# Kernel optimization log

Measured on AMD Instinct MI355X. Metric: run time of the kernel, lower is better.

Reference implementation:

```python
import jax, jax.numpy as jnp
import numpy as np

BN_EPS = 1e-5


def grid_sample_bilinear(img, grid):
    """Torch F.grid_sample, mode=bilinear, padding_mode=zeros, align_corners=False.
    img: (B, C, H, W); grid: (B, N, 2) in [-1, 1] -> (B, C, N)."""
    B, C, H, W = img.shape
    x = ((grid[..., 0] + 1.0) * W - 1.0) * 0.5  # (B, N) pixel coords
    y = ((grid[..., 1] + 1.0) * H - 1.0) * 0.5
    x0 = jnp.floor(x)
    y0 = jnp.floor(y)
    x1 = x0 + 1.0
    y1 = y0 + 1.0
    wx1 = x - x0
    wx0 = 1.0 - wx1
    wy1 = y - y0
    wy0 = 1.0 - wy1
    img_flat = img.reshape(B, C, H * W)

    def corner(xi, yi, w):
        valid = (xi >= 0) & (xi <= W - 1) & (yi >= 0) & (yi <= H - 1)
        xi_c = jnp.clip(xi, 0, W - 1).astype(jnp.int32)
        yi_c = jnp.clip(yi, 0, H - 1).astype(jnp.int32)
        idx = yi_c * W + xi_c  # (B, N)
        vals = jnp.take_along_axis(img_flat, idx[:, None, :], axis=2)  # (B, C, N)
        return vals * (w * valid.astype(img.dtype))[:, None, :]

    return (corner(x0, y0, wx0 * wy0) + corner(x1, y0, wx1 * wy0)
            + corner(x0, y1, wx0 * wy1) + corner(x1, y1, wx1 * wy1))


def conv1x1(x, w, b):
    # x: (B, Cin, N), w: (Cout, Cin), b: (Cout,)
    return jnp.einsum('oi,bin->bon', w, x) + b[None, :, None]


def batchnorm1d_train(x, gamma, beta):
    # training-mode BN over (batch, length) per channel, biased variance
    mean = jnp.mean(x, axis=(0, 2), keepdims=True)
    var = jnp.mean((x - mean) ** 2, axis=(0, 2), keepdims=True)
    xn = (x - mean) * jax.lax.rsqrt(var + BN_EPS)
    return xn * gamma[None, :, None] + beta[None, :, None]


def setup_inputs() -> dict:
    key = jax.random.key(0)
    ks = jax.random.split(key, 12)
    B, N, CI, CP, H, W, R = 4, 16384, 256, 256, 64, 160, 4
    Cin = CI + CP
    Cb = CP // R

    def glorot(k, shape):
        fan_in = shape[1]
        return jax.random.normal(k, shape, dtype=jnp.float32) * (1.0 / np.sqrt(fan_in))

    return {
        'pts_img': jax.random.uniform(ks[0], (B, N, 2), dtype=jnp.float32, minval=-1.0, maxval=1.0),
        'img_feats': jax.random.normal(ks[1], (B, CI, H, W), dtype=jnp.float32),
        'pts_feats': jax.random.normal(ks[2], (B, CP, N), dtype=jnp.float32),
        'fusion_w': glorot(ks[3], (CP, Cin)),
        'fusion_b': jax.random.normal(ks[4], (CP,), dtype=jnp.float32) * 0.01,
        'bn_gamma': jnp.ones((CP,), dtype=jnp.float32),
        'bn_beta': jnp.zeros((CP,), dtype=jnp.float32),
        'ca1_w': glorot(ks[5], (Cb, CP)),
        'ca1_b': jax.random.normal(ks[6], (Cb,), dtype=jnp.float32) * 0.01,
        'ca2_w': glorot(ks[7], (CP, Cb)),
        'ca2_b': jax.random.normal(ks[8], (CP,), dtype=jnp.float32) * 0.01,
        'sa_w': glorot(ks[9], (Cb, CP)),
        'sa_b': jax.random.normal(ks[10], (Cb,), dtype=jnp.float32) * 0.01,
    }


def reference(pts_img, img_feats, pts_feats, fusion_w, fusion_b, bn_gamma, bn_beta,
              ca1_w, ca1_b, ca2_w, ca2_b, sa_w, sa_b):
    # grid_sample gather: (B, C_I, N)
    pts_wise_img_feats = grid_sample_bilinear(img_feats, pts_img)
    fusion = jnp.concatenate([pts_wise_img_feats, pts_feats], axis=1)  # (B, C_I+C_P, N)
    # fusion MLP: conv1x1 + BN + ReLU
    fusion = jax.nn.relu(batchnorm1d_train(conv1x1(fusion, fusion_w, fusion_b), bn_gamma, bn_beta))
    # spatial attention: max over channels of bottleneck conv, sigmoid gate
    spatial = jax.nn.sigmoid(jnp.max(conv1x1(fusion, sa_w, sa_b), axis=1, keepdims=True))
    fusion = spatial * fusion
    # channel attention: bottleneck MLP, global max-pool over points, sigmoid gate
    ca = conv1x1(jax.nn.relu(conv1x1(fusion, ca1_w, ca1_b)), ca2_w, ca2_b)  # (B, C_P, N)
    channel = jax.nn.sigmoid(jnp.max(ca, axis=2, keepdims=True))  # (B, C_P, 1)
    return channel * fusion
```

## Files before the change

### kernel.cpp

```cpp
#include <hip/hip_runtime.h>
#include <stdint.h>


typedef __attribute__((ext_vector_type(8))) short bf16x8;
typedef __attribute__((ext_vector_type(4))) float f32x4;

#define B_ 4
#define N_ 16384
#define H_ 64
#define W_ 160
#define HW_ (H_ * W_)
#define K_ 512

__device__ __forceinline__ float bf2f(unsigned short u) {
    union { unsigned int i; float f; } c; c.i = ((unsigned int)u) << 16; return c.f;
}
__device__ __forceinline__ unsigned short f2bf(float f) {
    union { float f; unsigned int i; } c; c.f = f;
    unsigned int u = c.i;
    return (unsigned short)((u + 0x7FFFu + ((u >> 16) & 1u)) >> 16);
}
__device__ __forceinline__ unsigned int fkey(float f) {
    union { float f; unsigned int u; int i; } c; c.f = f;
    return (c.i < 0) ? ~c.u : (c.u | 0x80000000u);
}
__device__ __forceinline__ float funkey(unsigned int k) {
    union { unsigned int u; float f; } c;
    c.u = (k & 0x80000000u) ? (k & 0x7FFFFFFFu) : ~k;
    return c.f;
}

__device__ __forceinline__ void async_copy16(void* lds, const void* g) {
#if defined(__has_builtin) && __has_builtin(__builtin_amdgcn_global_load_lds)
    __builtin_amdgcn_global_load_lds(
        (const __attribute__((address_space(1))) unsigned int*)g,
        (__attribute__((address_space(3))) unsigned int*)lds, 16, 0, 0);
#else
    *(uint4*)lds = *(const uint4*)g;
#endif
}

__global__ __launch_bounds__(256) void k_init(const float* __restrict__ fw,
                                              const float* __restrict__ saw,
                                              const float* __restrict__ c1w,
                                              const float* __restrict__ c2w,
                                              unsigned short* WfB, unsigned short* saB,
                                              unsigned short* ca1B, unsigned short* ca2B,
                                              float* buckets, unsigned int* camax) {
    int t = threadIdx.x;
    int j = blockIdx.x;
    if (j == 0) {
        for (int i = t; i < 16 * 512; i += 256) buckets[i] = 0.f;
        for (int i = t; i < 8 * 1024; i += 256) camax[i] = 0u;
    }
    int i = j * 256 + t;
    if (i < 131072) WfB[i] = f2bf(fw[i]);
    else if (i < 147456) saB[i - 131072] = f2bf(saw[i - 131072]);
    else if (i < 163840) ca1B[i - 147456] = f2bf(c1w[i - 147456]);
    else if (i < 180224) ca2B[i - 163840] = f2bf(c2w[i - 163840]);
}

__global__ __launch_bounds__(256, 3) void k_zimg(const unsigned short* __restrict__ WfB,
                                                 const float* __restrict__ img,
                                                 unsigned short* __restrict__ ZT) {
    __shared__ __align__(16) char smem[33792];
    unsigned short* At = (unsigned short*)smem;
    unsigned short* Bt = (unsigned short*)(smem + 16384);
    unsigned short* tile = (unsigned short*)smem;

    int t = threadIdx.x;
    int hw0 = blockIdx.x * 64, b = blockIdx.y;
    int w = t >> 6, lane = t & 63, quad = lane >> 4, l15 = lane & 15;

    const f32x4 fzero = {0.f, 0.f, 0.f, 0.f};
    f32x4 acc[4][4];
#pragma unroll
    for (int i = 0; i < 4; ++i)
#pragma unroll
        for (int j = 0; j < 4; ++j) acc[i][j] = fzero;

    for (int kt = 0; kt < 8; ++kt) {
        int k0 = kt * 32;
        __syncthreads();
#pragma unroll
        for (int q = 0; q < 4; ++q) {
            int row = q * 64 + (t >> 2);
            async_copy16(At + (size_t)q * 2048 + (size_t)t * 8,
                         WfB + (size_t)row * K_ + k0 + (t & 3) * 8);
        }
        {
            int c_local = t & 31, g = t >> 5;
            int c = k0 + c_local;
            const float* src = img + ((size_t)b * 256 + c) * (size_t)HW_ + hw0 + g * 8;
            float4 v0 = *(const float4*)(src + 0);
            float4 v1 = *(const float4*)(src + 4);
            unsigned short* dst = Bt + (size_t)(g * 8) * 40 + c_local;
            dst[0 * 40] = f2bf(v0.x); dst[1 * 40] = f2bf(v0.y);
            dst[2 * 40] = f2bf(v0.z); dst[3 * 40] = f2bf(v0.w);
            dst[4 * 40] = f2bf(v1.x); dst[5 * 40] = f2bf(v1.y);
            dst[6 * 40] = f2bf(v1.z); dst[7 * 40] = f2bf(v1.w);
        }
        __syncthreads();
        bf16x8 af[4], bv[4];
#pragma unroll
        for (int j = 0; j < 4; ++j)
            bv[j] = *(const bf16x8*)(Bt + (j * 16 + l15) * 40 + quad * 8);
#pragma unroll
        for (int i = 0; i < 4; ++i)
            af[i] = *(const bf16x8*)(At + (w * 64 + i * 16 + l15) * 32 + quad * 8);
#pragma unroll
        for (int i = 0; i < 4; ++i)
#pragma unroll
            for (int j = 0; j < 4; ++j)
                acc[i][j] = __builtin_amdgcn_mfma_f32_16x16x32_bf16(af[i], bv[j], acc[i][j], 0, 0, 0);
    }

    __syncthreads();
#pragma unroll
    for (int i = 0; i < 4; ++i) {
        int m = w * 64 + i * 16 + quad * 4;
#pragma unroll
        for (int j = 0; j < 4; ++j) {
            int n = j * 16 + l15;
            ushort4 o;
            o.x = f2bf(acc[i][j][0]);
            o.y = f2bf(acc[i][j][1]);
            o.z = f2bf(acc[i][j][2]);
            o.w = f2bf(acc[i][j][3]);
            *(ushort4*)(tile + n * 264 + m) = o;
        }
    }
    __syncthreads();
    unsigned short* Zb = ZT + ((size_t)b * HW_ + hw0) * 256;
#pragma unroll
    for (int pass = 0; pass < 8; ++pass) {
        int row = pass * 8 + (t >> 5);
        int col = (t & 31) * 8;
        *(uint4*)(Zb + (size_t)row * 256 + col) = *(const uint4*)(tile + row * 264 + col);
    }
}

__global__ __launch_bounds__(256, 4) void k_gemm1p(const unsigned short* __restrict__ WfB,
                                                   const float* __restrict__ pim,
                                                   const unsigned short* __restrict__ ZT,
                                                   const float* __restrict__ pts,
                                                   const float* __restrict__ fb,
                                                   unsigned short* __restrict__ Y,
                                                   float* __restrict__ buckets) {
    __shared__ __align__(16) char smem[38912];
    unsigned short* At = (unsigned short*)smem;
    unsigned short* Bt = (unsigned short*)(smem + 16384);
    unsigned short* tile = (unsigned short*)smem;
    uint4*  offs4 = (uint4*)(smem + 33792);
    float4* wts4  = (float4*)(smem + 34816);
    float* biasS = (float*)(smem + 35840);
    float* redS  = (float*)(smem + 36864);
    float* redQ  = (float*)(smem + 37888);

    int t = threadIdx.x;
    int n0 = blockIdx.x * 64, bb = blockIdx.y;
    int w = t >> 6, lane = t & 63, quad = lane >> 4, l15 = lane & 15;
    const unsigned short* Zb = ZT + (size_t)bb * HW_ * 256;

    if (t < 64) {
        float2 g2 = *(const float2*)(pim + (size_t)((size_t)bb * N_ + n0 + t) * 2);
        float x = (g2.x + 1.0f) * (0.5f * W_) - 0.5f;
        float y = (g2.y + 1.0f) * (0.5f * H_) - 0.5f;
        float xf = floorf(x), yf = floorf(y);
        float wx1 = x - xf, wx0 = 1.0f - wx1;
        float wy1 = y - yf, wy0 = 1.0f - wy1;
        int x0 = (int)xf, y0 = (int)yf;
        int x1 = x0 + 1, y1 = y0 + 1;
        float vx0 = (x0 >= 0 && x0 < W_) ? 1.f : 0.f;
        float vx1 = (x1 >= 0 && x1 < W_) ? 1.f : 0.f;
        float vy0 = (y0 >= 0 && y0 < H_) ? 1.f : 0.f;
        float vy1 = (y1 >= 0 && y1 < H_) ? 1.f : 0.f;
        int cx0 = min(max(x0, 0), W_ - 1), cx1 = min(max(x1, 0), W_ - 1);
        int cy0 = min(max(y0, 0), H_ - 1), cy1 = min(max(y1, 0), H_ - 1);
        uint4 o4;
        o4.x = (unsigned)(cy0 * W_ + cx0);
        o4.y = (unsigned)(cy0 * W_ + cx1);
        o4.z = (unsigned)(cy1 * W_ + cx0);
        o4.w = (unsigned)(cy1 * W_ + cx1);
        offs4[t] = o4;
        float4 w4;
        w4.x = wx0 * wy0 * vx0 * vy0;
        w4.y = wx1 * wy0 * vx1 * vy0;
        w4.z = wx0 * wy1 * vx0 * vy1;
        w4.w = wx1 * wy1 * vx1 * vy1;
        wts4[t] = w4;
    }
    biasS[t] = fb[t];

    const f32x4 fzero = {0.f, 0.f, 0.f, 0.f};
    f32x4 acc[4][4];
#pragma unroll
    for (int i = 0; i < 4; ++i)
#pragma unroll
        for (int j = 0; j < 4; ++j) acc[i][j] = fzero;

    for (int kt = 0; kt < 8; ++kt) {
        int k0 = kt * 32;
        __syncthreads();
#pragma unroll
        for (int q = 0; q < 4; ++q) {
            int row = q * 64 + (t >> 2);
            async_copy16(At + (size_t)q * 2048 + (size_t)t * 8,
                         WfB + (size_t)row * K_ + 256 + k0 + (t & 3) * 8);
        }
        {
            int c_local = t & 31, g = t >> 5;
            int c = k0 + c_local;
            const float* src = pts + ((size_t)bb * 256 + c) * (size_t)N_ + n0 + g * 8;
            float4 v0 = *(const float4*)(src + 0);
            float4 v1 = *(const float4*)(src + 4);
            unsigned short* dst = Bt + (size_t)(g * 8) * 40 + c_local;
            dst[0 * 40] = f2bf(v0.x); dst[1 * 40] = f2bf(v0.y);
            dst[2 * 40] = f2bf(v0.z); dst[3 * 40] = f2bf(v0.w);
            dst[4 * 40] = f2bf(v1.x); dst[5 * 40] = f2bf(v1.y);
            dst[6 * 40] = f2bf(v1.z); dst[7 * 40] = f2bf(v1.w);
        }
        __syncthreads();
        bf16x8 af[4], bv[4];
#pragma unroll
        for (int j = 0; j < 4; ++j)
            bv[j] = *(const bf16x8*)(Bt + (j * 16 + l15) * 40 + quad * 8);
#pragma unroll
        for (int i = 0; i < 4; ++i)
            af[i] = *(const bf16x8*)(At + (w * 64 + i * 16 + l15) * 32 + quad * 8);
#pragma unroll
        for (int i = 0; i < 4; ++i)
#pragma unroll
            for (int j = 0; j < 4; ++j)
                acc[i][j] = __builtin_amdgcn_mfma_f32_16x16x32_bf16(af[i], bv[j], acc[i][j], 0, 0, 0);
    }

    __syncthreads();

    {
        int pt = t >> 2, q = t & 3;
        uint4 o4 = offs4[pt];
        float4 w4 = wts4[pt];
        const unsigned short* pA = Zb + (size_t)o4.x * 256;
        const unsigned short* pB = Zb + (size_t)o4.y * 256;
        const unsigned short* pC = Zb + (size_t)o4.z * 256;
        const unsigned short* pD = Zb + (size_t)o4.w * 256;
#pragma unroll
        for (int s = 0; s < 8; ++s) {
            int mc = q * 64 + s * 8;
            uint4 cA = *(const uint4*)(pA + mc);
            uint4 cB = *(const uint4*)(pB + mc);
            uint4 cC = *(const uint4*)(pC + mc);
            uint4 cD = *(const uint4*)(pD + mc);
            const unsigned short* qa = (const unsigned short*)&cA;
            const unsigned short* qb = (const unsigned short*)&cB;
            const unsigned short* qc = (const unsigned short*)&cC;
            const unsigned short* qd = (const unsigned short*)&cD;
            uint4 ov;
            unsigned short* po = (unsigned short*)&ov;
#pragma unroll
            for (int e = 0; e < 8; ++e)
                po[e] = f2bf(w4.x * bf2f(qa[e]) + w4.y * bf2f(qb[e]) +
                             w4.z * bf2f(qc[e]) + w4.w * bf2f(qd[e]));
            *(uint4*)(tile + pt * 264 + mc) = ov;
        }
    }
    __syncthreads();
#pragma unroll
    for (int i = 0; i < 4; ++i) {
        int mloc = w * 64 + i * 16 + quad * 4;
        float b0 = biasS[mloc + 0], b1 = biasS[mloc + 1];
        float b2 = biasS[mloc + 2], b3 = biasS[mloc + 3];
        float s0 = 0.f, q0 = 0.f, s1 = 0.f, q1 = 0.f;
        float s2 = 0.f, q2 = 0.f, s3 = 0.f, q3 = 0.f;
#pragma unroll
        for (int j = 0; j < 4; ++j) {
            int n = j * 16 + l15;
            ushort4 v = *(const ushort4*)(tile + n * 264 + mloc);
            float y0 = acc[i][j][0] + bf2f(v.x) + b0;
            float y1 = acc[i][j][1] + bf2f(v.y) + b1;
            float y2 = acc[i][j][2] + bf2f(v.z) + b2;
            float y3 = acc[i][j][3] + bf2f(v.w) + b3;
            s0 += y0; q0 += y0 * y0;
            s1 += y1; q1 += y1 * y1;
            s2 += y2; q2 += y2 * y2;
            s3 += y3; q3 += y3 * y3;
            ushort4 o;
            o.x = f2bf(y0); o.y = f2bf(y1); o.z = f2bf(y2); o.w = f2bf(y3);
            *(ushort4*)(tile + n * 264 + mloc) = o;
        }
#pragma unroll
        for (int d = 1; d < 16; d <<= 1) {
            s0 += __shfl_xor(s0, d, 64); q0 += __shfl_xor(q0, d, 64);
            s1 += __shfl_xor(s1, d, 64); q1 += __shfl_xor(q1, d, 64);
            s2 += __shfl_xor(s2, d, 64); q2 += __shfl_xor(q2, d, 64);
            s3 += __shfl_xor(s3, d, 64); q3 += __shfl_xor(q3, d, 64);
        }
        if (l15 == 0) {
            redS[mloc + 0] = s0; redQ[mloc + 0] = q0;
            redS[mloc + 1] = s1; redQ[mloc + 1] = q1;
            redS[mloc + 2] = s2; redQ[mloc + 2] = q2;
            redS[mloc + 3] = s3; redQ[mloc + 3] = q3;
        }
    }
    __syncthreads();
    {
        float* bk = buckets + (size_t)(blockIdx.x & 15) * 512;
        atomicAdd(bk + t, redS[t]);
        atomicAdd(bk + 256 + t, redQ[t]);
    }
    size_t Yrow0 = ((size_t)bb * N_ + n0) * 256;
#pragma unroll
    for (int pass = 0; pass < 8; ++pass) {
        int row = pass * 8 + (t >> 5);
        int col = (t & 31) * 8;
        *(uint4*)(Y + Yrow0 + (size_t)row * 256 + col) = *(const uint4*)(tile + row * 264 + col);
    }
}

__global__ __launch_bounds__(256, 2) void k_gate(const unsigned short* __restrict__ Y,
                                                 const float* __restrict__ buckets,
                                                 const float* __restrict__ gamma,
                                                 const float* __restrict__ beta,
                                                 const unsigned short* __restrict__ saB,
                                                 const float* __restrict__ sab,
                                                 const unsigned short* __restrict__ c1B,
                                                 const float* __restrict__ c1b,
                                                 const unsigned short* __restrict__ c2B,
                                                 unsigned int* __restrict__ camax,
                                                 float* __restrict__ sp_g,
                                                 float* __restrict__ ss_out) {
    __shared__ __align__(16) unsigned short Ft[64 * 264];
    __shared__ __align__(16) unsigned short Ht[64 * 72];
    __shared__ float scS[256], shS[256];
    __shared__ float saPart[4][64];
    __shared__ float spL[64];
    int t = threadIdx.x;
    size_t pts0 = (size_t)blockIdx.x * 64;
    int b = (int)(pts0 >> 14);
    int w = t >> 6, lane = t & 63, quad = lane >> 4, l15 = lane & 15;
    int jrow = w * 16 + l15;

    bf16x8 bvs[8], bvc[8];
#pragma unroll
    for (int kt = 0; kt < 8; ++kt) {
        bvs[kt] = *(const bf16x8*)(saB + (size_t)jrow * 256 + kt * 32 + quad * 8);
        bvc[kt] = *(const bf16x8*)(c1B + (size_t)jrow * 256 + kt * 32 + quad * 8);
    }
    float sbias = sab[jrow];
    float cbias = c1b[jrow];

    {
        float s = 0.f, q = 0.f;
#pragma unroll
        for (int bk = 0; bk < 16; ++bk) {
            s += buckets[bk * 512 + t];
            q += buckets[bk * 512 + 256 + t];
        }
        const float inv = 1.0f / (float)(B_ * N_);
        float mean = s * inv;
        float var = q * inv - mean * mean;
        float sc = gamma[t] * rsqrtf(var + 1e-5f);
        float sh = beta[t] - mean * sc;
        scS[t] = sc;
        shS[t] = sh;
        if (blockIdx.x == 0) { ss_out[t] = sc; ss_out[256 + t] = sh; }
    }
    __syncthreads();

    int cc = (t * 8) & 255;
    float scr[8], shr[8];
#pragma unroll
    for (int e = 0; e < 8; ++e) { scr[e] = scS[cc + e]; shr[e] = shS[cc + e]; }
    for (int idx = t * 8; idx < 64 * 256; idx += 2048) {
        int r = idx >> 8;
        uint4 v = *(const uint4*)(Y + (pts0 + r) * 256 + cc);
        unsigned short* us = (unsigned short*)&v;
#pragma unroll
        for (int e = 0; e < 8; ++e) {
            float f = bf2f(us[e]) * scr[e] + shr[e];
            us[e] = f2bf(fmaxf(f, 0.f));
        }
        *(uint4*)(Ft + r * 264 + cc) = v;
    }
    __syncthreads();

    const f32x4 fzero = {0.f, 0.f, 0.f, 0.f};
    f32x4 accS[4], accC[4];
#pragma unroll
    for (int i = 0; i < 4; ++i) { accS[i] = fzero; accC[i] = fzero; }
#pragma unroll
    for (int kt = 0; kt < 8; ++kt) {
        bf16x8 af[4];
#pragma unroll
        for (int i = 0; i < 4; ++i)
            af[i] = *(const bf16x8*)(Ft + (i * 16 + l15) * 264 + kt * 32 + quad * 8);
#pragma unroll
        for (int i = 0; i < 4; ++i) {
            accS[i] = __builtin_amdgcn_mfma_f32_16x16x32_bf16(af[i], bvs[kt], accS[i], 0, 0, 0);
            accC[i] = __builtin_amdgcn_mfma_f32_16x16x32_bf16(af[i], bvc[kt], accC[i], 0, 0, 0);
        }
    }
#pragma unroll
    for (int i = 0; i < 4; ++i) {
#pragma unroll
        for (int r = 0; r < 4; ++r) {
            float v = accS[i][r] + sbias;
#pragma unroll
            for (int d = 1; d < 16; d <<= 1) v = fmaxf(v, __shfl_xor(v, d, 64));
            if (l15 == 0) saPart[w][i * 16 + quad * 4 + r] = v;
        }
    }
    __syncthreads();
    if (t < 64) {
        float m4 = fmaxf(fmaxf(saPart[0][t], saPart[1][t]),
                         fmaxf(saPart[2][t], saPart[3][t]));
        float sv = 1.0f / (1.0f + __expf(-m4));
        spL[t] = sv;
        sp_g[pts0 + t] = sv;
    }
    __syncthreads();

#pragma unroll
    for (int i = 0; i < 4; ++i) {
#pragma unroll
        for (int r = 0; r < 4; ++r) {
            int pt = i * 16 + quad * 4 + r;
            float hv = fmaxf(accC[i][r] * spL[pt] + cbias, 0.f);
            Ht[pt * 72 + jrow] = f2bf(hv);
        }
    }
    __syncthreads();

    {
        bf16x8 b2a[4], b2b[4];
#pragma unroll
        for (int mt = 0; mt < 4; ++mt) {
            b2a[mt] = *(const bf16x8*)(c2B + (size_t)(w * 64 + mt * 16 + l15) * 64 + quad * 8);
            b2b[mt] = *(const bf16x8*)(c2B + (size_t)(w * 64 + mt * 16 + l15) * 64 + 32 + quad * 8);
        }
        float vmax[4] = {-3e38f, -3e38f, -3e38f, -3e38f};
#pragma unroll
        for (int i = 0; i < 4; ++i) {
            bf16x8 a0 = *(const bf16x8*)(Ht + (i * 16 + l15) * 72 + quad * 8);
            bf16x8 a1 = *(const bf16x8*)(Ht + (i * 16 + l15) * 72 + 32 + quad * 8);
#pragma unroll
            for (int mt = 0; mt < 4; ++mt) {
                f32x4 acc = __builtin_amdgcn_mfma_f32_16x16x32_bf16(a0, b2a[mt], fzero, 0, 0, 0);
                acc = __builtin_amdgcn_mfma_f32_16x16x32_bf16(a1, b2b[mt], acc, 0, 0, 0);
#pragma unroll
                for (int r = 0; r < 4; ++r) vmax[mt] = fmaxf(vmax[mt], acc[r]);
            }
        }
        unsigned int* cam = camax + (size_t)(blockIdx.x & 7) * 1024 + b * 256;
#pragma unroll
        for (int mt = 0; mt < 4; ++mt) {
            float v = vmax[mt];
            v = fmaxf(v, __shfl_xor(v, 16, 64));
            v = fmaxf(v, __shfl_xor(v, 32, 64));
            if (quad == 0) atomicMax(cam + w * 64 + mt * 16 + l15, fkey(v));
        }
    }
}

__global__ __launch_bounds__(256) void k_out(const unsigned short* __restrict__ Y,
                                             const unsigned int* __restrict__ camax,
                                             const float* __restrict__ c2b,
                                             const float* __restrict__ ss,
                                             const float* __restrict__ sp_g,
                                             float* __restrict__ out) {
    __shared__ __align__(16) unsigned short tile[64 * 68];
    __shared__ float ch[64], scT[64], shT[64], spT[64];
    int t = threadIdx.x;
    int n0 = blockIdx.x * 64, m0 = blockIdx.y * 64, b = blockIdx.z;
    if (t < 64) {
        int m = m0 + t;
        unsigned int k = 0u;
#pragma unroll
        for (int bk = 0; bk < 8; ++bk) k = max(k, camax[bk * 1024 + b * 256 + m]);
        ch[t] = 1.0f / (1.0f + __expf(-(funkey(k) + c2b[m])));
        scT[t] = ss[m];
        shT[t] = ss[256 + m];
        spT[t] = sp_g[(size_t)b * N_ + n0 + t];
    }
    int sub = (t & 15) * 4, grp = t >> 4;
    const unsigned short* src = Y + ((size_t)b * N_ + n0) * 256 + m0;
#pragma unroll
    for (int it = 0; it < 4; ++it) {
        int nl = grp + it * 16;
        ushort4 v = *(const ushort4*)(src + (size_t)nl * 256 + sub);
        *(ushort4*)(tile + nl * 68 + sub) = v;
    }
    __syncthreads();
    float* dst = out + ((size_t)b * 256 + m0) * N_ + n0;
#pragma unroll
    for (int it = 0; it < 4; ++it) {
        int ml = grp + it * 16;
        float g = ch[ml], scv = scT[ml], shv = shT[ml];
        float4 o;
        o.x = fmaxf(bf2f(tile[(sub + 0) * 68 + ml]) * scv + shv, 0.f) * spT[sub + 0] * g;
        o.y = fmaxf(bf2f(tile[(sub + 1) * 68 + ml]) * scv + shv, 0.f) * spT[sub + 1] * g;
        o.z = fmaxf(bf2f(tile[(sub + 2) * 68 + ml]) * scv + shv, 0.f) * spT[sub + 2] * g;
        o.w = fmaxf(bf2f(tile[(sub + 3) * 68 + ml]) * scv + shv, 0.f) * spT[sub + 3] * g;
        *(float4*)(dst + (size_t)ml * N_ + sub) = o;
    }
}

extern "C" void kernel_launch(void* const* d_in, const int* in_sizes, int n_in,
                              void* d_out, int out_size, void* d_ws, size_t ws_size,
                              hipStream_t stream) {
    (void)in_sizes; (void)n_in; (void)out_size; (void)ws_size;
    const float* pts_img = (const float*)d_in[0];
    const float* img     = (const float*)d_in[1];
    const float* pts     = (const float*)d_in[2];
    const float* fw      = (const float*)d_in[3];
    const float* fbias   = (const float*)d_in[4];
    const float* gamma   = (const float*)d_in[5];
    const float* beta    = (const float*)d_in[6];
    const float* c1w     = (const float*)d_in[7];
    const float* c1b     = (const float*)d_in[8];
    const float* c2w     = (const float*)d_in[9];
    const float* c2b     = (const float*)d_in[10];
    const float* saw     = (const float*)d_in[11];
    const float* sab     = (const float*)d_in[12];
    float* out = (float*)d_out;

    char* ws = (char*)d_ws;
    unsigned short* ZT   = (unsigned short*)(ws);
    unsigned short* Y    = (unsigned short*)(ws + 20971520);
    unsigned short* WfB  = (unsigned short*)(ws + 54525952);
    unsigned short* saB  = (unsigned short*)(ws + 54788096);
    unsigned short* ca1B = (unsigned short*)(ws + 54820864);
    unsigned short* ca2B = (unsigned short*)(ws + 54853632);
    float* buckets       = (float*)(ws + 54886400);
    unsigned int* camax  = (unsigned int*)(ws + 54919168);
    float* sp_g          = (float*)(ws + 54951936);
    float* ss            = (float*)(ws + 55214080);

    k_init<<<704, 256, 0, stream>>>(fw, saw, c1w, c2w, WfB, saB, ca1B, ca2B, buckets, camax);
    k_zimg<<<dim3(160, 4), 256, 0, stream>>>(WfB, img, ZT);
    k_gemm1p<<<dim3(256, 4), 256, 0, stream>>>(WfB, pts_img, ZT, pts, fbias, Y, buckets);
    k_gate<<<1024, 256, 0, stream>>>(Y, buckets, gamma, beta, saB, sab, ca1B, c1b,
                                     ca2B, camax, sp_g, ss);
    k_out<<<dim3(256, 4, 4), 256, 0, stream>>>(Y, camax, c2b, ss, sp_g, out);
}
```

Before: 299.9 us.

## Sort sample points by pixel bin before bilinear gather into separate blend kernel

Bilinear corner offsets and weights are now computed in a standalone kernel, and points are counting-sorted by their top-left pixel using a histogram, a single-block scan and an atomic scatter. A new blend kernel gathers the four ZT rows in sorted order, aiming for cache locality, and writes the blended image features to Y. The GEMM kernel then reloads those features from Y instead of gathering them inline. This adds four launches, a serial single-block scan over 40960 bins, and an extra global round trip of the blended tile.

```diff
diff --git a/kernel.cpp b/kernel.cpp
--- a/kernel.cpp
+++ b/kernel.cpp
@@ -11,6 +11,7 @@
 #define W_ 160
 #define HW_ (H_ * W_)
 #define K_ 512
+#define NBIN_ (B_ * HW_)
 
 __device__ __forceinline__ float bf2f(unsigned short u) {
     union { unsigned int i; float f; } c; c.i = ((unsigned int)u) << 16; return c.f;
@@ -46,18 +47,88 @@
                                               const float* __restrict__ c2w,
                                               unsigned short* WfB, unsigned short* saB,
                                               unsigned short* ca1B, unsigned short* ca2B,
-                                              float* buckets, unsigned int* camax) {
+                                              float* buckets, unsigned int* camax,
+                                              unsigned int* hist) {
     int t = threadIdx.x;
     int j = blockIdx.x;
     if (j == 0) {
         for (int i = t; i < 16 * 512; i += 256) buckets[i] = 0.f;
         for (int i = t; i < 8 * 1024; i += 256) camax[i] = 0u;
     }
+    if (j < 160) hist[j * 256 + t] = 0u;
     int i = j * 256 + t;
     if (i < 131072) WfB[i] = f2bf(fw[i]);
     else if (i < 147456) saB[i - 131072] = f2bf(saw[i - 131072]);
     else if (i < 163840) ca1B[i - 147456] = f2bf(c1w[i - 147456]);
     else if (i < 180224) ca2B[i - 163840] = f2bf(c2w[i - 163840]);
+}
+
+__global__ __launch_bounds__(256) void k_corners(const float* __restrict__ pim,
+                                                 uint4* __restrict__ offs4A,
+                                                 float4* __restrict__ wts4A,
+                                                 unsigned int* __restrict__ hist) {
+    int idx = blockIdx.x * 256 + threadIdx.x;
+    float2 g2 = *(const float2*)(pim + (size_t)idx * 2);
+    float x = (g2.x + 1.0f) * (0.5f * W_) - 0.5f;
+    float y = (g2.y + 1.0f) * (0.5f * H_) - 0.5f;
+    float xf = floorf(x), yf = floorf(y);
+    float wx1 = x - xf, wx0 = 1.0f - wx1;
+    float wy1 = y - yf, wy0 = 1.0f - wy1;
+    int x0 = (int)xf, y0 = (int)yf;
+    int x1 = x0 + 1, y1 = y0 + 1;
+    float vx0 = (x0 >= 0 && x0 < W_) ? 1.f : 0.f;
+    float vx1 = (x1 >= 0 && x1 < W_) ? 1.f : 0.f;
+    float vy0 = (y0 >= 0 && y0 < H_) ? 1.f : 0.f;
+    float vy1 = (y1 >= 0 && y1 < H_) ? 1.f : 0.f;
+    int cx0 = min(max(x0, 0), W_ - 1), cx1 = min(max(x1, 0), W_ - 1);
+    int cy0 = min(max(y0, 0), H_ - 1), cy1 = min(max(y1, 0), H_ - 1);
+    uint4 o4;
+    o4.x = (unsigned)(cy0 * W_ + cx0);
+    o4.y = (unsigned)(cy0 * W_ + cx1);
+    o4.z = (unsigned)(cy1 * W_ + cx0);
+    o4.w = (unsigned)(cy1 * W_ + cx1);
+    offs4A[idx] = o4;
+    float4 w4;
+    w4.x = wx0 * wy0 * vx0 * vy0;
+    w4.y = wx1 * wy0 * vx1 * vy0;
+    w4.z = wx0 * wy1 * vx0 * vy1;
+    w4.w = wx1 * wy1 * vx1 * vy1;
+    wts4A[idx] = w4;
+    int b = idx >> 14;
+    atomicAdd(&hist[b * HW_ + (int)o4.x], 1u);
+}
+
+__global__ __launch_bounds__(256) void k_scan(const unsigned int* __restrict__ hist,
+                                              unsigned int* __restrict__ binOfs) {
+    __shared__ unsigned int sums[256];
+    int t = threadIdx.x;
+    const int CH = NBIN_ / 256;
+    unsigned int s = 0;
+    for (int j = 0; j < CH; ++j) s += hist[t * CH + j];
+    sums[t] = s;
+    __syncthreads();
+    for (int d = 1; d < 256; d <<= 1) {
+        unsigned int v = (t >= d) ? sums[t - d] : 0u;
+        __syncthreads();
+        sums[t] += v;
+        __syncthreads();
+    }
+    unsigned int base = (t == 0) ? 0u : sums[t - 1];
+    for (int j = 0; j < CH; ++j) {
+        unsigned int h = hist[t * CH + j];
+        binOfs[t * CH + j] = base;
+        base += h;
+    }
+}
+
+__global__ __launch_bounds__(256) void k_scatter(const uint4* __restrict__ offs4A,
+                                                 unsigned int* __restrict__ binOfs,
+                                                 unsigned int* __restrict__ perm) {
+    int idx = blockIdx.x * 256 + threadIdx.x;
+    int b = idx >> 14;
+    unsigned int key = offs4A[idx].x;
+    unsigned int r = atomicAdd(&binOfs[b * HW_ + key], 1u);
+    perm[r] = (unsigned int)idx;
 }
 
 __global__ __launch_bounds__(256, 3) void k_zimg(const unsigned short* __restrict__ WfB,
@@ -140,56 +211,65 @@
     }
 }
 
+__global__ __launch_bounds__(256) void k_blend(const unsigned int* __restrict__ perm,
+                                               const uint4* __restrict__ offs4A,
+                                               const float4* __restrict__ wts4A,
+                                               const unsigned short* __restrict__ ZT,
+                                               unsigned short* __restrict__ Y) {
+    int t = threadIdx.x;
+    int bl = blockIdx.x;
+    int q = t & 3;
+#pragma unroll
+    for (int p = 0; p < 2; ++p) {
+        int rank = bl * 128 + p * 64 + (t >> 2);
+        unsigned int idx = perm[rank];
+        int b = (int)(idx >> 14), n = (int)(idx & 16383);
+        uint4 o4 = offs4A[idx];
+        float4 w4 = wts4A[idx];
+        const unsigned short* Zb = ZT + (size_t)b * HW_ * 256;
+        const unsigned short* pA = Zb + (size_t)o4.x * 256 + q * 64;
+        const unsigned short* pB = Zb + (size_t)o4.y * 256 + q * 64;
+        const unsigned short* pC = Zb + (size_t)o4.z * 256 + q * 64;
+        const unsigned short* pD = Zb + (size_t)o4.w * 256 + q * 64;
+        unsigned short* dst = Y + ((size_t)b * N_ + n) * 256 + q * 64;
+#pragma unroll
+        for (int s = 0; s < 8; ++s) {
+            uint4 cA = *(const uint4*)(pA + s * 8);
+            uint4 cB = *(const uint4*)(pB + s * 8);
+            uint4 cC = *(const uint4*)(pC + s * 8);
+            uint4 cD = *(const uint4*)(pD + s * 8);
+            const unsigned short* qa = (const unsigned short*)&cA;
+            const unsigned short* qb = (const unsigned short*)&cB;
+            const unsigned short* qc = (const unsigned short*)&cC;
+            const unsigned short* qd = (const unsigned short*)&cD;
+            uint4 ov;
+            unsigned short* po = (unsigned short*)&ov;
+#pragma unroll
+            for (int e = 0; e < 8; ++e)
+                po[e] = f2bf(w4.x * bf2f(qa[e]) + w4.y * bf2f(qb[e]) +
+                             w4.z * bf2f(qc[e]) + w4.w * bf2f(qd[e]));
+            *(uint4*)(dst + s * 8) = ov;
+        }
+    }
+}
+
 __global__ __launch_bounds__(256, 4) void k_gemm1p(const unsigned short* __restrict__ WfB,
-                                                   const float* __restrict__ pim,
-                                                   const unsigned short* __restrict__ ZT,
                                                    const float* __restrict__ pts,
                                                    const float* __restrict__ fb,
                                                    unsigned short* __restrict__ Y,
                                                    float* __restrict__ buckets) {
-    __shared__ __align__(16) char smem[38912];
+    __shared__ __align__(16) char smem[36864];
     unsigned short* At = (unsigned short*)smem;
     unsigned short* Bt = (unsigned short*)(smem + 16384);
     unsigned short* tile = (unsigned short*)smem;
-    uint4*  offs4 = (uint4*)(smem + 33792);
-    float4* wts4  = (float4*)(smem + 34816);
-    float* biasS = (float*)(smem + 35840);
-    float* redS  = (float*)(smem + 36864);
-    float* redQ  = (float*)(smem + 37888);
+    float* biasS = (float*)(smem + 33792);
+    float* redS  = (float*)(smem + 34816);
+    float* redQ  = (float*)(smem + 35840);
 
     int t = threadIdx.x;
     int n0 = blockIdx.x * 64, bb = blockIdx.y;
     int w = t >> 6, lane = t & 63, quad = lane >> 4, l15 = lane & 15;
-    const unsigned short* Zb = ZT + (size_t)bb * HW_ * 256;
-
-    if (t < 64) {
-        float2 g2 = *(const float2*)(pim + (size_t)((size_t)bb * N_ + n0 + t) * 2);
-        float x = (g2.x + 1.0f) * (0.5f * W_) - 0.5f;
-        float y = (g2.y + 1.0f) * (0.5f * H_) - 0.5f;
-        float xf = floorf(x), yf = floorf(y);
-        float wx1 = x - xf, wx0 = 1.0f - wx1;
-        float wy1 = y - yf, wy0 = 1.0f - wy1;
-        int x0 = (int)xf, y0 = (int)yf;
-        int x1 = x0 + 1, y1 = y0 + 1;
-        float vx0 = (x0 >= 0 && x0 < W_) ? 1.f : 0.f;
-        float vx1 = (x1 >= 0 && x1 < W_) ? 1.f : 0.f;
-        float vy0 = (y0 >= 0 && y0 < H_) ? 1.f : 0.f;
-        float vy1 = (y1 >= 0 && y1 < H_) ? 1.f : 0.f;
-        int cx0 = min(max(x0, 0), W_ - 1), cx1 = min(max(x1, 0), W_ - 1);
-        int cy0 = min(max(y0, 0), H_ - 1), cy1 = min(max(y1, 0), H_ - 1);
-        uint4 o4;
-        o4.x = (unsigned)(cy0 * W_ + cx0);
-        o4.y = (unsigned)(cy0 * W_ + cx1);
-        o4.z = (unsigned)(cy1 * W_ + cx0);
-        o4.w = (unsigned)(cy1 * W_ + cx1);
-        offs4[t] = o4;
-        float4 w4;
-        w4.x = wx0 * wy0 * vx0 * vy0;
-        w4.y = wx1 * wy0 * vx1 * vy0;
-        w4.z = wx0 * wy1 * vx0 * vy1;
-        w4.w = wx1 * wy1 * vx1 * vy1;
-        wts4[t] = w4;
-    }
+
     biasS[t] = fb[t];
 
     const f32x4 fzero = {0.f, 0.f, 0.f, 0.f};
@@ -237,33 +317,12 @@
 
     __syncthreads();
 
-    {
-        int pt = t >> 2, q = t & 3;
-        uint4 o4 = offs4[pt];
-        float4 w4 = wts4[pt];
-        const unsigned short* pA = Zb + (size_t)o4.x * 256;
-        const unsigned short* pB = Zb + (size_t)o4.y * 256;
-        const unsigned short* pC = Zb + (size_t)o4.z * 256;
-        const unsigned short* pD = Zb + (size_t)o4.w * 256;
-#pragma unroll
-        for (int s = 0; s < 8; ++s) {
-            int mc = q * 64 + s * 8;
-            uint4 cA = *(const uint4*)(pA + mc);
-            uint4 cB = *(const uint4*)(pB + mc);
-            uint4 cC = *(const uint4*)(pC + mc);
-            uint4 cD = *(const uint4*)(pD + mc);
-            const unsigned short* qa = (const unsigned short*)&cA;
-            const unsigned short* qb = (const unsigned short*)&cB;
-            const unsigned short* qc = (const unsigned short*)&cC;
-            const unsigned short* qd = (const unsigned short*)&cD;
-            uint4 ov;
-            unsigned short* po = (unsigned short*)&ov;
-#pragma unroll
-            for (int e = 0; e < 8; ++e)
-                po[e] = f2bf(w4.x * bf2f(qa[e]) + w4.y * bf2f(qb[e]) +
-                             w4.z * bf2f(qc[e]) + w4.w * bf2f(qd[e]));
-            *(uint4*)(tile + pt * 264 + mc) = ov;
-        }
+    size_t Yrow0 = ((size_t)bb * N_ + n0) * 256;
+#pragma unroll
+    for (int pass = 0; pass < 8; ++pass) {
+        int row = pass * 8 + (t >> 5);
+        int col = (t & 31) * 8;
+        *(uint4*)(tile + row * 264 + col) = *(const uint4*)(Y + Yrow0 + (size_t)row * 256 + col);
     }
     __syncthreads();
 #pragma unroll
@@ -309,7 +368,6 @@
         atomicAdd(bk + t, redS[t]);
         atomicAdd(bk + 256 + t, redQ[t]);
     }
-    size_t Yrow0 = ((size_t)bb * N_ + n0) * 256;
 #pragma unroll
     for (int pass = 0; pass < 8; ++pass) {
         int row = pass * 8 + (t >> 5);
@@ -536,10 +594,20 @@
     unsigned int* camax  = (unsigned int*)(ws + 54919168);
     float* sp_g          = (float*)(ws + 54951936);
     float* ss            = (float*)(ws + 55214080);
-
-    k_init<<<704, 256, 0, stream>>>(fw, saw, c1w, c2w, WfB, saB, ca1B, ca2B, buckets, camax);
+    uint4* offs4A        = (uint4*)(ws + 55216128);
+    float4* wts4A        = (float4*)(ws + 56264704);
+    unsigned int* hist   = (unsigned int*)(ws + 57313280);
+    unsigned int* binOfs = (unsigned int*)(ws + 57477120);
+    unsigned int* perm   = (unsigned int*)(ws + 57640960);
+
+    k_init<<<704, 256, 0, stream>>>(fw, saw, c1w, c2w, WfB, saB, ca1B, ca2B,
+                                    buckets, camax, hist);
+    k_corners<<<256, 256, 0, stream>>>(pts_img, offs4A, wts4A, hist);
     k_zimg<<<dim3(160, 4), 256, 0, stream>>>(WfB, img, ZT);
-    k_gemm1p<<<dim3(256, 4), 256, 0, stream>>>(WfB, pts_img, ZT, pts, fbias, Y, buckets);
+    k_scan<<<1, 256, 0, stream>>>(hist, binOfs);
+    k_scatter<<<256, 256, 0, stream>>>(offs4A, binOfs, perm);
+    k_blend<<<512, 256, 0, stream>>>(perm, offs4A, wts4A, ZT, Y);
+    k_gemm1p<<<dim3(256, 4), 256, 0, stream>>>(WfB, pts, fbias, Y, buckets);
     k_gate<<<1024, 256, 0, stream>>>(Y, buckets, gamma, beta, saB, sab, ca1B, c1b,
                                      ca2B, camax, sp_g, ss);
     k_out<<<dim3(256, 4, 4), 256, 0, stream>>>(Y, camax, c2b, ss, sp_g, out);
```

Result: slower. 330.3 us (+10.2%).
